# Performance work log

Hardware: AMD Instinct MI355X
Metric: run time of the kernel (lower is better)

Reference implementation:

```python
import jax, jax.numpy as jnp
import numpy as np

ALPHA = 0.5
BETA = 5.0
LOGIT_SCALE = 100.0  # exp(log(100)) -- CLIP's learned logit scale at its clamp value
NUM_CLASSES = 200


def _l2norm(x):
    return x / jnp.linalg.norm(x, axis=-1, keepdims=True)


def setup_inputs() -> dict:
    key = jax.random.key(0)
    k1, k2, k3, k4 = jax.random.split(key, 4)
    img_f = jax.random.normal(k1, (1024, 512), dtype=jnp.float32)
    text_features = jax.random.normal(k2, (200, 512), dtype=jnp.float32)
    keys = jax.random.normal(k3, (50000, 512), dtype=jnp.float32)
    labels = jax.random.randint(k4, (50000,), 0, NUM_CLASSES, dtype=jnp.int64)
    return {"img_f": img_f, "text_features": text_features, "keys": keys, "labels": labels}


def reference(img_f, text_features, keys, labels):
    # encode_image output is L2-normalized in the module; keys were built from
    # normalized image features, text_features are normalized class embeddings.
    q = _l2norm(img_f)            # [B, D]
    t = _l2norm(text_features)    # [C, D]
    k = _l2norm(keys)             # [N, D]

    # CLIP zero-shot branch: scale * q @ t.T -> [B, C]
    z = LOGIT_SCALE * jnp.einsum('bd,cd->bc', q, t)

    # Tip-Adapter cache branch: exp(beta * q @ keys.T) @ one_hot(labels)
    sim = jnp.einsum('bd,nd->bn', q, k)                 # [B, N]
    aff = jnp.exp(BETA * sim)                           # [B, N]
    values = jax.nn.one_hot(labels, NUM_CLASSES, dtype=aff.dtype)  # [N, C]
    c = aff @ values                                    # [B, C]

    return (1.0 - ALPHA) * z + ALPHA * c
```

## Files before the change

### kernel.cpp

```cpp
#include <hip/hip_runtime.h>

#define B_Q    1024
#define D_K    512
#define N_CLS  200
#define N_KEYS 50000
#define N_PAD  50048
#define N_EXT  (N_PAD + 256)
#define N_ZT   (N_PAD / 128)

typedef __attribute__((ext_vector_type(8))) short bf16x8;
typedef __attribute__((ext_vector_type(4))) float f32x4;

__device__ __forceinline__ unsigned short f2bf(float f) {
  union { float f; unsigned int i; } v; v.f = f;
  unsigned int r = v.i + 0x7fffu + ((v.i >> 16) & 1u);
  return (unsigned short)(r >> 16);
}
__device__ __forceinline__ uint4 pack8(const float f[8], float s) {
  uint4 o;
  o.x = (unsigned)f2bf(f[0]*s) | ((unsigned)f2bf(f[1]*s) << 16);
  o.y = (unsigned)f2bf(f[2]*s) | ((unsigned)f2bf(f[3]*s) << 16);
  o.z = (unsigned)f2bf(f[4]*s) | ((unsigned)f2bf(f[5]*s) << 16);
  o.w = (unsigned)f2bf(f[6]*s) | ((unsigned)f2bf(f[7]*s) << 16);
  return o;
}
__device__ __forceinline__ void async_copy16(const void* g, void* lds) {
  __builtin_amdgcn_global_load_lds(
      (const __attribute__((address_space(1))) unsigned int*)g,
      (__attribute__((address_space(3))) unsigned int*)lds, 16, 0, 0);
}

__global__ void k_hist(const int* __restrict__ labels, int* __restrict__ hist) {
  __shared__ int h[N_CLS];
  int t = threadIdx.x;
  if (t < N_CLS) h[t] = 0;
  __syncthreads();
  int n = blockIdx.x * 256 + t;
  if (n < N_KEYS) atomicAdd(&h[labels[n]], 1);
  __syncthreads();
  if (t < N_CLS && h[t]) atomicAdd(&hist[t], h[t]);
}

__global__ void k_scan(const int* __restrict__ hist, int* __restrict__ cursor) {
  __shared__ int s[N_CLS];
  int t = threadIdx.x;
  int v = (t < N_CLS) ? hist[t] : 0;
  if (t < N_CLS) s[t] = v;
  __syncthreads();
  for (int d = 1; d < N_CLS; d <<= 1) {
    int x = 0;
    if (t < N_CLS && t >= d) x = s[t - d];
    __syncthreads();
    if (t < N_CLS) s[t] += x;
    __syncthreads();
  }
  if (t < N_CLS) cursor[t] = s[t] - v;
}

__global__ void k_perm(const int* __restrict__ labels, int* __restrict__ cursor,
                       int* __restrict__ dest) {
  __shared__ int lh[N_CLS];
  __shared__ int lbase[N_CLS];
  int t = threadIdx.x;
  if (t < N_CLS) lh[t] = 0;
  __syncthreads();
  int n = blockIdx.x * 256 + t;
  bool valid = (n < N_KEYS);
  int l = 0, lo = 0;
  if (valid) { l = labels[n]; lo = atomicAdd(&lh[l], 1); }
  __syncthreads();
  if (t < N_CLS && lh[t] > 0) lbase[t] = atomicAdd(&cursor[t], lh[t]);
  __syncthreads();
  if (valid) dest[n] = lbase[l] + lo;
}

__global__ void k_prep2(const float* __restrict__ keys, const float* __restrict__ img,
                        const float* __restrict__ txt, const int* __restrict__ labels,
                        const int* __restrict__ dest, unsigned short* __restrict__ qn,
                        unsigned short* __restrict__ kn, int* __restrict__ cls) {
  int w = threadIdx.x >> 6, lane = threadIdx.x & 63;
  int row = blockIdx.x * 4 + w;
  const float* src; unsigned short* dst; int r;
  if (row < N_PAD) {
    if (row >= N_KEYS) {
      *((uint4*)(kn + (size_t)row * D_K) + lane) = make_uint4(0, 0, 0, 0);
      if (lane == 0) cls[row] = N_CLS;
      return;
    }
    int d = dest[row];
    if (lane == 0) cls[d] = labels[row];
    src = keys + (size_t)row * D_K;
    dst = kn + (size_t)d * D_K;
  } else if (row < N_PAD + B_Q) {
    r = row - N_PAD;
    src = img + (size_t)r * D_K;
    dst = qn + (size_t)r * D_K;
  } else if (row < N_PAD + B_Q + N_CLS) {
    r = row - N_PAD - B_Q;
    src = txt + (size_t)r * D_K;
    dst = kn + (size_t)(N_PAD + r) * D_K;
  } else if (row < N_PAD + B_Q + N_CLS + 56) {
    r = N_PAD + N_CLS + (row - N_PAD - B_Q - N_CLS);
    *((uint4*)(kn + (size_t)r * D_K) + lane) = make_uint4(0, 0, 0, 0);
    return;
  } else return;
  const float4* s4 = (const float4*)src + lane * 2;
  float4 a = s4[0], b = s4[1];
  float f[8] = {a.x, a.y, a.z, a.w, b.x, b.y, b.z, b.w};
  float ss = 0.f;
#pragma unroll
  for (int i = 0; i < 8; i++) ss += f[i] * f[i];
#pragma unroll
  for (int d = 1; d < 64; d <<= 1) ss += __shfl_xor(ss, d);
  float rinv = rsqrtf(ss);
  *((uint4*)dst + lane) = pack8(f, rinv);
}

__global__ __launch_bounds__(256, 2) void k_main(const unsigned short* __restrict__ qn,
                                                 const unsigned short* __restrict__ kn,
                                                 const int* __restrict__ cls,
                                                 float* __restrict__ out) {
  __shared__ unsigned short As[2][128 * 64];
  __shared__ unsigned short Bs[2][128 * 64];
  int t = threadIdx.x;
  int tileB = blockIdx.x, tileN = blockIdx.y;
  int rowB0 = tileB * 128, rowN0 = tileN * 128;

  f32x4 acc[4][4];
#pragma unroll
  for (int i = 0; i < 4; i++)
#pragma unroll
    for (int j = 0; j < 4; j++) acc[i][j] = (f32x4){0.f, 0.f, 0.f, 0.f};

  int lane = t & 63, w = t >> 6;
  int wr = (w >> 1) * 64, wc = (w & 1) * 64;
  int l15 = lane & 15, lq = lane >> 4;
  const int rA = t >> 3;
  const int gsw = ((t & 7) ^ (rA & 7)) * 8;
  const int sw = l15 & 7;

#pragma unroll
  for (int i = 0; i < 4; i++) {
    int row = i * 32 + rA;
    async_copy16(qn + (size_t)(rowB0 + row) * D_K + gsw, &As[0][i * 2048 + t * 8]);
    async_copy16(kn + (size_t)(rowN0 + row) * D_K + gsw, &Bs[0][i * 2048 + t * 8]);
  }

  for (int kt = 0; kt < 8; kt++) {
    int cur = kt & 1;
    __syncthreads();
    if (kt < 7) {
      int nxt = cur ^ 1, k0 = (kt + 1) * 64;
#pragma unroll
      for (int i = 0; i < 4; i++) {
        int row = i * 32 + rA;
        async_copy16(qn + (size_t)(rowB0 + row) * D_K + k0 + gsw, &As[nxt][i * 2048 + t * 8]);
        async_copy16(kn + (size_t)(rowN0 + row) * D_K + k0 + gsw, &Bs[nxt][i * 2048 + t * 8]);
      }
    }
#pragma unroll
    for (int ks = 0; ks < 64; ks += 32) {
      bf16x8 af[4], bf[4];
#pragma unroll
      for (int i = 0; i < 4; i++)
        af[i] = *(const bf16x8*)&As[cur][(wr + 16 * i + l15) * 64 + ((((ks >> 3) + lq) ^ sw) * 8)];
#pragma unroll
      for (int j = 0; j < 4; j++)
        bf[j] = *(const bf16x8*)&Bs[cur][(wc + 16 * j + l15) * 64 + ((((ks >> 3) + lq) ^ sw) * 8)];
#pragma unroll
      for (int i = 0; i < 4; i++)
#pragma unroll
        for (int j = 0; j < 4; j++)
          acc[i][j] = __builtin_amdgcn_mfma_f32_16x16x32_bf16(af[i], bf[j], acc[i][j], 0, 0, 0);
    }
  }

  if (tileN >= N_ZT) {
#pragma unroll
    for (int i = 0; i < 4; i++)
#pragma unroll
      for (int j = 0; j < 4; j++) {
        int col = rowN0 + wc + 16 * j + l15 - N_PAD;
        if (col < N_CLS) {
#pragma unroll
          for (int r = 0; r < 4; r++) {
            int row = rowB0 + wr + 16 * i + lq * 4 + r;
            atomicAdd(out + (size_t)row * N_CLS + col, 50.0f * acc[i][j][r]);
          }
        }
      }
    return;
  }

#pragma unroll
  for (int i = 0; i < 4; i++)
#pragma unroll
    for (int j = 0; j < 4; j++)
#pragma unroll
      for (int r = 0; r < 4; r++) acc[i][j][r] = __expf(5.0f * acc[i][j][r]);

  int cj[4];
#pragma unroll
  for (int j = 0; j < 4; j++) cj[j] = cls[rowN0 + wc + 16 * j + l15];
  int cseg0 = cls[rowN0 + wc];
  int cseg1 = cls[rowN0 + wc + 63];

  for (int c = cseg0; c <= cseg1; c++) {
    if (c >= N_CLS) break;
#pragma unroll
    for (int i = 0; i < 4; i++) {
      float s0 = 0.f, s1 = 0.f, s2 = 0.f, s3 = 0.f;
#pragma unroll
      for (int j = 0; j < 4; j++) {
        if (cj[j] == c) {
          s0 += acc[i][j][0]; s1 += acc[i][j][1];
          s2 += acc[i][j][2]; s3 += acc[i][j][3];
        }
      }
#pragma unroll
      for (int d = 1; d < 16; d <<= 1) {
        s0 += __shfl_xor(s0, d); s1 += __shfl_xor(s1, d);
        s2 += __shfl_xor(s2, d); s3 += __shfl_xor(s3, d);
      }
      if (l15 == 0) {
        int row = rowB0 + wr + 16 * i + lq * 4;
        float* o = out + (size_t)row * N_CLS + c;
        if (s0 != 0.f) atomicAdd(o + 0 * N_CLS, 0.5f * s0);
        if (s1 != 0.f) atomicAdd(o + 1 * N_CLS, 0.5f * s1);
        if (s2 != 0.f) atomicAdd(o + 2 * N_CLS, 0.5f * s2);
        if (s3 != 0.f) atomicAdd(o + 3 * N_CLS, 0.5f * s3);
      }
    }
  }
}

extern "C" void kernel_launch(void* const* d_in, const int* in_sizes, int n_in,
                              void* d_out, int out_size, void* d_ws, size_t ws_size,
                              hipStream_t stream) {
  (void)in_sizes; (void)n_in; (void)out_size; (void)ws_size;
  const float* img    = (const float*)d_in[0];
  const float* txt    = (const float*)d_in[1];
  const float* keys   = (const float*)d_in[2];
  const int*   labels = (const int*)d_in[3];
  float*       out    = (float*)d_out;

  char* ws = (char*)d_ws;
  unsigned short* qn = (unsigned short*)(ws + 0);
  unsigned short* kn = (unsigned short*)(ws + 1048576);
  int*  dest   = (int*)(ws + 52559872);
  int*  cls    = (int*)(ws + 52760064);
  int*  hist   = (int*)(ws + 52960256);
  int*  cursor = (int*)(ws + 52961280);

  hipMemsetAsync(hist, 0, 256 * sizeof(int), stream);
  hipMemsetAsync(out, 0, (size_t)B_Q * N_CLS * sizeof(float), stream);

  k_hist<<<196, 256, 0, stream>>>(labels, hist);
  k_scan<<<1, 256, 0, stream>>>(hist, cursor);
  k_perm<<<196, 256, 0, stream>>>(labels, cursor, dest);
  k_prep2<<<(N_PAD + B_Q + N_CLS + 56 + 3) / 4, 256, 0, stream>>>(
      keys, img, txt, labels, dest, qn, kn, cls);
  k_main<<<dim3(B_Q / 128, N_ZT + 2), 256, 0, stream>>>(qn, kn, cls, out);
}
```

Measured before the change: 297.4 us.

## Load key tile directly from global into registers and fuse hist/scan kernels

The main GEMM kernel stops staging the key operand through LDS and instead reads each wave's B fragments directly from global memory into registers. Only the query tile stays double-buffered in LDS, and launch bounds rise to three blocks per CU. The histogram and scan kernels are merged using a last-block-done atomic counter, which removes one launch. Direct global loads of B drop LDS traffic and capacity but add global latency that is no longer overlapped by async prefetch, and they lose cross-wave reuse of the shared B tile.

```diff
diff --git a/kernel.cpp b/kernel.cpp
--- a/kernel.cpp
+++ b/kernel.cpp
@@ -30,8 +30,10 @@
       (__attribute__((address_space(3))) unsigned int*)lds, 16, 0, 0);
 }
 
-__global__ void k_hist(const int* __restrict__ labels, int* __restrict__ hist) {
+__global__ void k_histscan(const int* __restrict__ labels, int* __restrict__ hist,
+                           int* __restrict__ cursor) {
   __shared__ int h[N_CLS];
+  __shared__ int lastFlag;
   int t = threadIdx.x;
   if (t < N_CLS) h[t] = 0;
   __syncthreads();
@@ -39,13 +41,13 @@
   if (n < N_KEYS) atomicAdd(&h[labels[n]], 1);
   __syncthreads();
   if (t < N_CLS && h[t]) atomicAdd(&hist[t], h[t]);
-}
-
-__global__ void k_scan(const int* __restrict__ hist, int* __restrict__ cursor) {
+  __threadfence();
+  if (t == 0) lastFlag = (atomicAdd(&hist[255], 1) == (int)gridDim.x - 1);
+  __syncthreads();
+  if (!lastFlag) return;
   __shared__ int s[N_CLS];
-  int t = threadIdx.x;
-  int v = (t < N_CLS) ? hist[t] : 0;
-  if (t < N_CLS) s[t] = v;
+  int v = 0;
+  if (t < N_CLS) { v = atomicAdd(&hist[t], 0); s[t] = v; }
   __syncthreads();
   for (int d = 1; d < N_CLS; d <<= 1) {
     int x = 0;
@@ -116,12 +118,11 @@
   *((uint4*)dst + lane) = pack8(f, rinv);
 }
 
-__global__ __launch_bounds__(256, 2) void k_main(const unsigned short* __restrict__ qn,
+__global__ __launch_bounds__(256, 3) void k_main(const unsigned short* __restrict__ qn,
                                                  const unsigned short* __restrict__ kn,
                                                  const int* __restrict__ cls,
                                                  float* __restrict__ out) {
   __shared__ unsigned short As[2][128 * 64];
-  __shared__ unsigned short Bs[2][128 * 64];
   int t = threadIdx.x;
   int tileB = blockIdx.x, tileN = blockIdx.y;
   int rowB0 = tileB * 128, rowN0 = tileN * 128;
@@ -139,34 +140,35 @@
   const int gsw = ((t & 7) ^ (rA & 7)) * 8;
   const int sw = l15 & 7;
 
-#pragma unroll
-  for (int i = 0; i < 4; i++) {
-    int row = i * 32 + rA;
-    async_copy16(qn + (size_t)(rowB0 + row) * D_K + gsw, &As[0][i * 2048 + t * 8]);
-    async_copy16(kn + (size_t)(rowN0 + row) * D_K + gsw, &Bs[0][i * 2048 + t * 8]);
-  }
+  const unsigned short* bptr[4];
+#pragma unroll
+  for (int j = 0; j < 4; j++)
+    bptr[j] = kn + (size_t)(rowN0 + wc + 16 * j + l15) * D_K + lq * 8;
+
+#pragma unroll
+  for (int i = 0; i < 4; i++)
+    async_copy16(qn + (size_t)(rowB0 + i * 32 + rA) * D_K + gsw, &As[0][i * 2048 + t * 8]);
 
   for (int kt = 0; kt < 8; kt++) {
     int cur = kt & 1;
     __syncthreads();
     if (kt < 7) {
-      int nxt = cur ^ 1, k0 = (kt + 1) * 64;
-#pragma unroll
-      for (int i = 0; i < 4; i++) {
-        int row = i * 32 + rA;
-        async_copy16(qn + (size_t)(rowB0 + row) * D_K + k0 + gsw, &As[nxt][i * 2048 + t * 8]);
-        async_copy16(kn + (size_t)(rowN0 + row) * D_K + k0 + gsw, &Bs[nxt][i * 2048 + t * 8]);
-      }
-    }
+      int k0n = (kt + 1) * 64;
+#pragma unroll
+      for (int i = 0; i < 4; i++)
+        async_copy16(qn + (size_t)(rowB0 + i * 32 + rA) * D_K + k0n + gsw,
+                     &As[cur ^ 1][i * 2048 + t * 8]);
+    }
+    int k0 = kt * 64;
 #pragma unroll
     for (int ks = 0; ks < 64; ks += 32) {
       bf16x8 af[4], bf[4];
 #pragma unroll
+      for (int j = 0; j < 4; j++)
+        bf[j] = *(const bf16x8*)(bptr[j] + k0 + ks);
+#pragma unroll
       for (int i = 0; i < 4; i++)
         af[i] = *(const bf16x8*)&As[cur][(wr + 16 * i + l15) * 64 + ((((ks >> 3) + lq) ^ sw) * 8)];
-#pragma unroll
-      for (int j = 0; j < 4; j++)
-        bf[j] = *(const bf16x8*)&Bs[cur][(wc + 16 * j + l15) * 64 + ((((ks >> 3) + lq) ^ sw) * 8)];
 #pragma unroll
       for (int i = 0; i < 4; i++)
 #pragma unroll
@@ -255,8 +257,7 @@
   hipMemsetAsync(hist, 0, 256 * sizeof(int), stream);
   hipMemsetAsync(out, 0, (size_t)B_Q * N_CLS * sizeof(float), stream);
 
-  k_hist<<<196, 256, 0, stream>>>(labels, hist);
-  k_scan<<<1, 256, 0, stream>>>(hist, cursor);
+  k_histscan<<<196, 256, 0, stream>>>(labels, hist, cursor);
   k_perm<<<196, 256, 0, stream>>>(labels, cursor, dest);
   k_prep2<<<(N_PAD + B_Q + N_CLS + 56 + 3) / 4, 256, 0, stream>>>(
       keys, img, txt, labels, dest, qn, kn, cls);
```

After: 314.6 us. 5.8% more time.
